# Kernel tuning notes

Hardware: AMD Instinct MI355X
Metric: run time of the kernel (lower is better)

## Reference

```python
import jax, jax.numpy as jnp
import numpy as np

T, B, S, H, E, V = 100, 64, 602, 1024, 512, 10000


def setup_inputs() -> dict:
    key = jax.random.key(0)
    ks = jax.random.split(key, 12)
    s = 0.02  # small init scale for numerical stability through tanh/sigmoid
    return {
        "tgt": jax.random.randint(ks[0], (T, B, 1), 0, V),
        "memory_bank": jax.random.normal(ks[1], (S, B, H), jnp.float32),
        "h0": jax.random.normal(ks[2], (2, B, H), jnp.float32) * 0.1,
        "c0": jax.random.normal(ks[3], (2, B, H), jnp.float32) * 0.1,
        "embedding": jax.random.normal(ks[4], (V, E), jnp.float32) * s,
        "Wi0": jax.random.normal(ks[5], (4 * H, E + H), jnp.float32) * s,
        "Wh0": jax.random.normal(ks[6], (4 * H, H), jnp.float32) * s,
        "bi0": jnp.zeros((4 * H,), jnp.float32),
        "bh0": jnp.zeros((4 * H,), jnp.float32),
        "Wi1": jax.random.normal(ks[7], (4 * H, H), jnp.float32) * s,
        "Wh1": jax.random.normal(ks[8], (4 * H, H), jnp.float32) * s,
        "bi1": jnp.zeros((4 * H,), jnp.float32),
        "bh1": jnp.zeros((4 * H,), jnp.float32),
        "W_attn": jax.random.normal(ks[9], (H, H), jnp.float32) * s,
        "W_out": jax.random.normal(ks[10], (H, 2 * H), jnp.float32) * s,
    }


def _lstm_cell(x, h, c, Wi, Wh, bi, bh):
    # PyTorch LSTM gate order: i, f, g, o
    g = x @ Wi.T + h @ Wh.T + bi + bh
    i, f, gg, o = jnp.split(g, 4, axis=-1)
    c2 = jax.nn.sigmoid(f) * c + jax.nn.sigmoid(i) * jnp.tanh(gg)
    h2 = jax.nn.sigmoid(o) * jnp.tanh(c2)
    return h2, c2


def reference(tgt, memory_bank, h0, c0, embedding, Wi0, Wh0, bi0, bh0,
              Wi1, Wh1, bi1, bh1, W_attn, W_out):
    emb = embedding[tgt[:, :, 0]]            # [T, B, E]
    M = jnp.transpose(memory_bank, (1, 0, 2))  # [B, S, H]

    def step(carry, e_t):
        hl0, hl1, cl0, cl1, feed = carry
        x = jnp.concatenate([e_t, feed], axis=-1)        # input feeding
        nh0, nc0 = _lstm_cell(x, hl0, cl0, Wi0, Wh0, bi0, bh0)
        nh1, nc1 = _lstm_cell(nh0, hl1, cl1, Wi1, Wh1, bi1, bh1)
        # GlobalAttention 'general': score = (h W) . m
        q = nh1 @ W_attn.T                                # [B, H]
        align = jnp.einsum('bh,bsh->bs', q, M)            # [B, S]
        a = jax.nn.softmax(align, axis=-1)
        ctx = jnp.einsum('bs,bsh->bh', a, M)              # [B, H]
        out = jnp.tanh(jnp.concatenate([ctx, nh1], -1) @ W_out.T)  # attn_h
        return (nh0, nh1, nc0, nc1, out), (out, a)

    init = (h0[0], h0[1], c0[0], c0[1], jnp.zeros((B, H), emb.dtype))
    (_, _, _, _, _), (outs, attns) = jax.lax.scan(step, init, emb)
    return outs, attns  # [T,B,H], [T,B,S]
```

## Files before the change

### kernel.cpp

```cpp
#include <hip/hip_runtime.h>


#define DI __device__ __forceinline__

typedef __attribute__((ext_vector_type(4))) short s4v;
typedef __attribute__((ext_vector_type(8))) short s8v;
typedef __attribute__((ext_vector_type(4))) float f4v;

DI float b2f(short u) {
  unsigned int x = ((unsigned int)(unsigned short)u) << 16;
  float f; __builtin_memcpy(&f, &x, 4); return f;
}
DI short f2b(float f) {
  unsigned int x; __builtin_memcpy(&x, &f, 4);
  return (short)((x + 0x7fffu + ((x >> 16) & 1u)) >> 16);
}
DI s8v cat8(s4v lo, s4v hi) {
  s8v r; r[0]=lo[0];r[1]=lo[1];r[2]=lo[2];r[3]=lo[3];
  r[4]=hi[0];r[5]=hi[1];r[6]=hi[2];r[7]=hi[3]; return r;
}
DI f4v mfma16(s8v a, s8v b, f4v c) {
  return __builtin_amdgcn_mfma_f32_16x16x32_bf16(a, b, c, 0, 0, 0);
}
DI float sigm(float x) { return 1.f / (1.f + __expf(-x)); }

DI unsigned long long ld64c(const void* p) {
  return __hip_atomic_load((const unsigned long long*)p, __ATOMIC_RELAXED,
                           __HIP_MEMORY_SCOPE_SYSTEM);
}
DI void st64c(void* p, unsigned long long v) {
  __hip_atomic_store((unsigned long long*)p, v, __ATOMIC_RELAXED,
                     __HIP_MEMORY_SCOPE_SYSTEM);
}
DI float ldfc(const float* p) {
  return __hip_atomic_load(p, __ATOMIC_RELAXED, __HIP_MEMORY_SCOPE_SYSTEM);
}
DI void stfc(float* p, float v) {
  __hip_atomic_store(p, v, __ATOMIC_RELAXED, __HIP_MEMORY_SCOPE_SYSTEM);
}
DI int ld32c(const int* p) {
  return __hip_atomic_load(p, __ATOMIC_RELAXED, __HIP_MEMORY_SCOPE_SYSTEM);
}
DI void st32c(int* p, int v) {
  __hip_atomic_store(p, v, __ATOMIC_RELAXED, __HIP_MEMORY_SCOPE_SYSTEM);
}
DI void st16c(short* p, short v) {
  asm volatile("global_store_short %0, %1, off sc0 sc1"
               :: "v"(p), "v"((unsigned int)(unsigned short)v) : "memory");
}
union U64S { unsigned long long u; short s[4]; };
union U64F { unsigned long long u; float f[2]; };


__global__ void cvt_bf16(const float* __restrict__ src, short* __restrict__ dst, long n8) {
  long i = (long)blockIdx.x * blockDim.x + threadIdx.x;
  long stride = (long)gridDim.x * blockDim.x;
  for (; i < n8; i += stride) {
    const float* s = src + i * 8;
    s8v o;
    #pragma unroll
    for (int j = 0; j < 8; ++j) o[j] = f2b(s[j]);
    *(s8v*)(dst + i * 8) = o;
  }
}

__global__ void pack_w(const float* __restrict__ WA, int Ka,
                       const float* __restrict__ WB, int Kb,
                       short* __restrict__ dst, int N, long total) {
  long i = (long)blockIdx.x * blockDim.x + threadIdx.x;
  long stride = (long)gridDim.x * blockDim.x;
  for (; i < total; i += stride) {
    int c = (int)(i & 3);
    long r = i >> 2;
    int n = (int)(r % N);
    int kt = (int)(r / N);
    int k = kt * 32 + c * 8;
    const float* s = (k < Ka) ? (WA + (size_t)n * Ka + k)
                              : (WB + (size_t)n * Kb + (k - Ka));
    s8v o;
    #pragma unroll
    for (int j = 0; j < 8; ++j) o[j] = f2b(s[j]);
    *(s8v*)(dst + r * 32 + c * 8) = o;
  }
}

__global__ __launch_bounds__(64) void emb_gather(const int* __restrict__ tgt,
                                                 const float* __restrict__ emb,
                                                 short* __restrict__ dst) {
  int tb = blockIdx.x;
  int idx = tgt[tb];
  const float* s = emb + (size_t)idx * 512 + threadIdx.x * 8;
  s8v o;
  #pragma unroll
  for (int j = 0; j < 8; ++j) o[j] = f2b(s[j]);
  *(s8v*)(dst + (size_t)tb * 512 + threadIdx.x * 8) = o;
}

__global__ void init_state(const float* __restrict__ h0, const float* __restrict__ c0,
                           short* __restrict__ h0r, short* __restrict__ h1r,
                           float* __restrict__ c0buf, float* __restrict__ c1buf,
                           short* __restrict__ feedr) {
  int i = blockIdx.x * 256 + threadIdx.x;
  if (i < 65536) {
    h0r[i] = f2b(h0[i]);
    h1r[i] = f2b(h0[65536 + i]);
    int row = i >> 10, col = i & 1023;
    size_t coff = (size_t)((row >> 4) * 64 + (col >> 4)) * 256
                + (row & 15) * 16 + (col & 15);
    c0buf[coff] = c0[i];
    c1buf[coff] = c0[65536 + i];
    feedr[i] = 0;
  }
}


template <int NG>
DI void kloop(const short* __restrict__ A, int ld, int nkt,
              const short* __restrict__ Wp, size_t wkt,
              f4v* acc, int rA, int g) {
  if (nkt <= 0) return;
  const short* ap = A + (size_t)rA * ld + 4 * g;
  s4v alo = *(const s4v*)ap, ahi = *(const s4v*)(ap + 16);
  s4v blo[NG], bhi[NG];
  #pragma unroll
  for (int t = 0; t < NG; ++t) {
    blo[t] = *(const s4v*)(Wp + (size_t)t * 32768);
    bhi[t] = *(const s4v*)(Wp + (size_t)t * 32768 + 16);
  }
  for (int kt = 0; kt < nkt - 1; ++kt) {
    const short* apn = ap + (kt + 1) * 32;
    const short* bpn = Wp + (size_t)(kt + 1) * wkt;
    s4v nalo = *(const s4v*)apn, nahi = *(const s4v*)(apn + 16);
    s4v nblo[NG], nbhi[NG];
    #pragma unroll
    for (int t = 0; t < NG; ++t) {
      nblo[t] = *(const s4v*)(bpn + (size_t)t * 32768);
      nbhi[t] = *(const s4v*)(bpn + (size_t)t * 32768 + 16);
    }
    s8v a = cat8(alo, ahi);
    #pragma unroll
    for (int t = 0; t < NG; ++t) acc[t] = mfma16(a, cat8(blo[t], bhi[t]), acc[t]);
    alo = nalo; ahi = nahi;
    #pragma unroll
    for (int t = 0; t < NG; ++t) { blo[t] = nblo[t]; bhi[t] = nbhi[t]; }
  }
  s8v a = cat8(alo, ahi);
  #pragma unroll
  for (int t = 0; t < NG; ++t) acc[t] = mfma16(a, cat8(blo[t], bhi[t]), acc[t]);
}

template <int NG>
DI void seg_gemm(const short* __restrict__ A0, int ld0, int n0,
                 const short* __restrict__ A1, int ld1, int n1,
                 const short* __restrict__ A2, int ld2, int n2,
                 const short* __restrict__ wbase, size_t wkt,
                 int k0, int k1, f4v* acc, int rA, int g) {
  int s = 0;
  {
    int a = k0 > s ? k0 : s, b = k1 < (s + n0) ? k1 : (s + n0);
    if (a < b) kloop<NG>(A0 + (size_t)(a - s) * 32, ld0, b - a,
                         wbase + (size_t)a * wkt, wkt, acc, rA, g);
    s += n0;
  }
  {
    int a = k0 > s ? k0 : s, b = k1 < (s + n1) ? k1 : (s + n1);
    if (a < b) kloop<NG>(A1 + (size_t)(a - s) * 32, ld1, b - a,
                         wbase + (size_t)a * wkt, wkt, acc, rA, g);
    s += n1;
  }
  if (n2 > 0) {
    int a = k0 > s ? k0 : s, b = k1 < (s + n2) ? k1 : (s + n2);
    if (a < b) kloop<NG>(A2 + (size_t)(a - s) * 32, ld2, b - a,
                         wbase + (size_t)a * wkt, wkt, acc, rA, g);
  }
}

template <int NG>
DI void wave_reduce(f4v* acc, float* smem, int w, int l) {
  #pragma unroll
  for (int t4 = 0; t4 < NG; ++t4)
    *(f4v*)&smem[(w * 64 + l) * 20 + t4 * 4] = acc[t4];
  __syncthreads();
  if (w == 0) {
    #pragma unroll
    for (int t4 = 0; t4 < NG; ++t4) {
      f4v s0 = *(f4v*)&smem[l * 20 + t4 * 4];
      #pragma unroll
      for (int ww = 1; ww < 4; ++ww) {
        f4v v = *(f4v*)&smem[(ww * 64 + l) * 20 + t4 * 4];
        #pragma unroll
        for (int j = 0; j < 4; ++j) s0[j] += v[j];
      }
      acc[t4] = s0;
    }
  }
}


DI void post(int* slot, int val) {
  if (threadIdx.x == 0) st32c(slot, val);
}
DI void wait64(const int* slots, int want) {
  for (;;) {
    int ok = 1;
    if (threadIdx.x < 64) ok = (ld32c(slots + threadIdx.x * 16) >= want);
    if (__syncthreads_and(ok)) break;
    __builtin_amdgcn_s_sleep(4);
  }
}
DI void wait4(const int* slots, int want) {
  for (;;) {
    int ok = 1;
    if (threadIdx.x < 4) ok = (ld32c(slots + threadIdx.x * 16) >= want);
    if (__syncthreads_and(ok)) break;
    __builtin_amdgcn_s_sleep(2);
  }
}


__global__ __launch_bounds__(256, 1) void decoder_k(
    const short* __restrict__ W0p, const short* __restrict__ W1p,
    const short* __restrict__ Wop, const short* __restrict__ Wap,
    const short* __restrict__ emba,
    const float* __restrict__ bi0, const float* __restrict__ bh0,
    const float* __restrict__ bi1, const float* __restrict__ bh1,
    short* h0r, short* h1r, short* feedr, short* ctxr, short* qb,
    float* c0b, float* c1b, float* alg, float* part, float* csum,
    const short* __restrict__ Mb, const float* __restrict__ memf,
    float* out, int useMb, int* bar) {
  __shared__ float smem[5248];
  const int bid = blockIdx.x, tid = threadIdx.x;
  const int w = tid >> 6, l = tid & 63, r15 = l & 15, g = l >> 4;
  const int cs = bid & 63, rt = bid >> 6;
  const int b = bid & 63, chunk = bid >> 6;
  int* s_p1 = bar;
  int* s_p2 = bar + 4096;
  int* s_p3 = bar + 8192;
  int* s_p6 = bar + 12288;
  int* s_p4 = bar + 16384;
  int* s_mg = bar + 20480;
  int* my_gemm_slot = bar ;
  f4v z = {0.f, 0.f, 0.f, 0.f};
  (void)my_gemm_slot;

  for (int t = 0; t < 100; ++t) {
    const size_t scur = (size_t)t * 65536, snxt = (size_t)(t + 1) * 65536;

    {
      wait64(s_p6 + rt * 1024, t);
      f4v acc[4] = {z, z, z, z};
      const short* wbase = W0p + (size_t)(cs * 16 + r15) * 32 + 4 * g;
      seg_gemm<4>(emba + (size_t)t * 64 * 512, 512, 16,
                  feedr + scur, 1024, 32, h0r + scur, 1024, 32,
                  wbase, (size_t)4096 * 32, w * 20, w * 20 + 20,
                  acc, rt * 16 + r15, g);
      wave_reduce<4>(acc, smem, w, l);
      if (w == 0) {
        int h = cs * 16 + r15;
        float bs0 = bi0[h] + bh0[h];
        float bs1 = bi0[1024 + h] + bh0[1024 + h];
        float bs2 = bi0[2048 + h] + bh0[2048 + h];
        float bs3 = bi0[3072 + h] + bh0[3072 + h];
        #pragma unroll
        for (int q = 0; q < 4; ++q) {
          int brow = rt * 16 + g * 4 + q;
          size_t off = (size_t)brow * 1024 + h;
          size_t coff = (size_t)bid * 256 + (g * 4 + q) * 16 + r15;
          float iv = acc[0][q] + bs0, fv = acc[1][q] + bs1;
          float gv = acc[2][q] + bs2, ov = acc[3][q] + bs3;
          float cn = sigm(fv) * c0b[coff] + sigm(iv) * tanhf(gv);
          float hn = sigm(ov) * tanhf(cn);
          c0b[coff] = cn;
          st16c(h0r + snxt + off, f2b(hn));
        }
      }
      __syncthreads();
      post(s_p1 + (rt * 64 + cs) * 16, t + 1);
    }

    {
      wait64(s_p1 + rt * 1024, t + 1);
      f4v acc[4] = {z, z, z, z};
      const short* wbase = W1p + (size_t)(cs * 16 + r15) * 32 + 4 * g;
      seg_gemm<4>(h0r + snxt, 1024, 32, h1r + scur, 1024, 32,
                  (const short*)nullptr, 0, 0,
                  wbase, (size_t)4096 * 32, w * 16, w * 16 + 16,
                  acc, rt * 16 + r15, g);
      wave_reduce<4>(acc, smem, w, l);
      if (w == 0) {
        int h = cs * 16 + r15;
        float bs0 = bi1[h] + bh1[h];
        float bs1 = bi1[1024 + h] + bh1[1024 + h];
        float bs2 = bi1[2048 + h] + bh1[2048 + h];
        float bs3 = bi1[3072 + h] + bh1[3072 + h];
        #pragma unroll
        for (int q = 0; q < 4; ++q) {
          int brow = rt * 16 + g * 4 + q;
          size_t off = (size_t)brow * 1024 + h;
          size_t coff = (size_t)bid * 256 + (g * 4 + q) * 16 + r15;
          float iv = acc[0][q] + bs0, fv = acc[1][q] + bs1;
          float gv = acc[2][q] + bs2, ov = acc[3][q] + bs3;
          float cn = sigm(fv) * c1b[coff] + sigm(iv) * tanhf(gv);
          float hn = sigm(ov) * tanhf(cn);
          c1b[coff] = cn;
          st16c(h1r + snxt + off, f2b(hn));
        }
      }
      __syncthreads();
      post(s_p2 + (rt * 64 + cs) * 16, t + 1);
    }

    {
      wait64(s_p2 + rt * 1024, t + 1);
      f4v acc[1] = {z};
      const short* wbase = Wap + (size_t)(cs * 16 + r15) * 32 + 4 * g;
      seg_gemm<1>(h1r + snxt, 1024, 32, (const short*)nullptr, 0, 0,
                  (const short*)nullptr, 0, 0,
                  wbase, (size_t)1024 * 32, w * 8, w * 8 + 8,
                  acc, rt * 16 + r15, g);
      wave_reduce<1>(acc, smem, w, l);
      if (w == 0) {
        int nb = cs * 16 + r15;
        #pragma unroll
        for (int q = 0; q < 4; ++q) {
          int brow = rt * 16 + g * 4 + q;
          st16c(qb + (size_t)brow * 1024 + nb, f2b(acc[0][q]));
        }
      }
      __syncthreads();
      post(s_p3 + (rt * 64 + cs) * 16, t + 1);
    }

    {
      wait64(s_p3 + (b >> 4) * 1024, t + 1);
      wait4(s_mg + b * 64, t);
      int s0 = chunk * 151;
      int send = 602 < s0 + 151 ? 602 : s0 + 151;
      const short* qp = qb + (size_t)b * 1024 + l * 16;
      float qf[16];
      #pragma unroll
      for (int c4 = 0; c4 < 4; ++c4) {
        U64S x; x.u = ld64c(qp + c4 * 4);
        #pragma unroll
        for (int j = 0; j < 4; ++j) qf[c4 * 4 + j] = b2f(x.s[j]);
      }
      float o[16];
      #pragma unroll
      for (int j = 0; j < 16; ++j) o[j] = 0.f;
      float ls8 = 0.f;
      for (int s = s0 + w; s < send; s += 16) {
        int sr[4] = {s, s + 4, s + 8, s + 12};
        bool has[4];
        #pragma unroll
        for (int r = 0; r < 4; ++r) has[r] = sr[r] < send;
        float mv[4][16];
        if (useMb) {
          #pragma unroll
          for (int r = 0; r < 4; ++r) {
            int sx = has[r] ? sr[r] : s;
            const short* mp = Mb + ((size_t)sx * 64 + b) * 1024 + l * 16;
            s8v a0 = *(const s8v*)mp, a1 = *(const s8v*)(mp + 8);
            #pragma unroll
            for (int j = 0; j < 8; ++j) {
              mv[r][j] = b2f(a0[j]); mv[r][8 + j] = b2f(a1[j]);
            }
          }
        } else {
          #pragma unroll
          for (int r = 0; r < 4; ++r) {
            int sx = has[r] ? sr[r] : s;
            const float* mp = memf + ((size_t)sx * 64 + b) * 1024 + l * 16;
            f4v a0 = *(const f4v*)mp, a1 = *(const f4v*)(mp + 4);
            f4v a2 = *(const f4v*)(mp + 8), a3 = *(const f4v*)(mp + 12);
            #pragma unroll
            for (int j = 0; j < 4; ++j) {
              mv[r][j] = a0[j]; mv[r][4 + j] = a1[j];
              mv[r][8 + j] = a2[j]; mv[r][12 + j] = a3[j];
            }
          }
        }
        float d[4] = {0.f, 0.f, 0.f, 0.f};
        #pragma unroll
        for (int j = 0; j < 16; ++j) {
          #pragma unroll
          for (int r = 0; r < 4; ++r) d[r] += qf[j] * mv[r][j];
        }
        #pragma unroll
        for (int off = 32; off; off >>= 1) {
          #pragma unroll
          for (int r = 0; r < 4; ++r) d[r] += __shfl_down(d[r], off);
        }
        float p[4];
        #pragma unroll
        for (int r = 0; r < 4; ++r) {
          d[r] = __shfl(d[r], 0);
          p[r] = has[r] ? __expf(fminf(d[r], 80.f) - 8.f) : 0.f;
          ls8 += p[r];
        }
        if (l == 0) {
          #pragma unroll
          for (int r = 0; r < 4; ++r)
            if (has[r]) stfc(alg + b * 602 + sr[r], p[r]);
        }
        #pragma unroll
        for (int j = 0; j < 16; ++j)
          o[j] += p[0] * mv[0][j] + p[1] * mv[1][j]
                + p[2] * mv[2][j] + p[3] * mv[3][j];
      }
      float* pp = part + (size_t)(b * 16 + chunk * 4 + w) * 1024;
      #pragma unroll
      for (int j4 = 0; j4 < 8; ++j4) {
        U64F x; x.f[0] = o[j4 * 2]; x.f[1] = o[j4 * 2 + 1];
        st64c(pp + l * 16 + j4 * 2, x.u);
      }
      if (l == 0) smem[5120 + w] = ls8;
      __syncthreads();
      if (tid == 0)
        stfc(csum + b * 4 + chunk,
             smem[5120] + smem[5121] + smem[5122] + smem[5123]);
      __syncthreads();
      post(s_p4 + (b * 4 + chunk) * 16, t + 1);
      wait4(s_p4 + b * 64, t + 1);
      {
        const float* cs4 = csum + b * 4;
        float L8 = ldfc(cs4) + ldfc(cs4 + 1) + ldfc(cs4 + 2) + ldfc(cs4 + 3);
        float invL = 1.f / L8;
        if (tid < 128) {
          int h = chunk * 256 + tid * 2;
          float a0 = 0.f, a1 = 0.f;
          #pragma unroll
          for (int p = 0; p < 16; ++p) {
            U64F x; x.u = ld64c(part + (size_t)(b * 16 + p) * 1024 + h);
            a0 += x.f[0]; a1 += x.f[1];
          }
          short* cp = ctxr + snxt + (size_t)b * 1024 + h;
          st16c(cp, f2b(a0 * invL));
          st16c(cp + 1, f2b(a1 * invL));
        }
        float* attns = out + 6553600 + (size_t)t * 64 * 602;
        for (int i = s0 + tid; i < send; i += 256)
          stfc(attns + b * 602 + i, ldfc(alg + b * 602 + i) * invL);
      }
      __syncthreads();
      post(s_mg + (b * 4 + chunk) * 16, t + 1);
    }

    {
      wait64(s_mg + rt * 1024, t + 1);
      f4v acc[1] = {z};
      const short* wbase = Wop + (size_t)(cs * 16 + r15) * 32 + 4 * g;
      seg_gemm<1>(ctxr + snxt, 1024, 32, h1r + snxt, 1024, 32,
                  (const short*)nullptr, 0, 0,
                  wbase, (size_t)1024 * 32, w * 16, w * 16 + 16,
                  acc, rt * 16 + r15, g);
      wave_reduce<1>(acc, smem, w, l);
      if (w == 0) {
        int nb = cs * 16 + r15;
        float* outp = out + (size_t)t * 65536;
        #pragma unroll
        for (int q = 0; q < 4; ++q) {
          int brow = rt * 16 + g * 4 + q;
          size_t off = (size_t)brow * 1024 + nb;
          float v = tanhf(acc[0][q]);
          stfc(outp + off, v);
          st16c(feedr + snxt + off, f2b(v));
        }
      }
      __syncthreads();
      post(s_p6 + (rt * 64 + cs) * 16, t + 1);
    }
  }
}


extern "C" void kernel_launch(void* const* d_in, const int* in_sizes, int n_in,
                              void* d_out, int out_size, void* d_ws, size_t ws_size,
                              hipStream_t stream) {
  const int*   tgt  = (const int*)  d_in[0];
  const float* mem  = (const float*)d_in[1];
  const float* h0   = (const float*)d_in[2];
  const float* c0   = (const float*)d_in[3];
  const float* embw = (const float*)d_in[4];
  const float* Wi0  = (const float*)d_in[5];
  const float* Wh0  = (const float*)d_in[6];
  const float* bi0  = (const float*)d_in[7];
  const float* bh0  = (const float*)d_in[8];
  const float* Wi1  = (const float*)d_in[9];
  const float* Wh1  = (const float*)d_in[10];
  const float* bi1  = (const float*)d_in[11];
  const float* bh1  = (const float*)d_in[12];
  const float* Wat  = (const float*)d_in[13];
  const float* Wou  = (const float*)d_in[14];
  float* out = (float*)d_out;

  char* base = (char*)d_ws;
  size_t off = 0;
  auto alloc = [&](size_t bytes) -> void* {
    void* p = base + off;
    off += (bytes + 255) & ~(size_t)255;
    return p;
  };
  const size_t RING = (size_t)101 * 65536;
  int* bar = (int*)alloc(131072);
  short* qb   = (short*)alloc(65536 * 2);
  float* csum = (float*)alloc(64 * 4 * 4);
  float* c0b  = (float*)alloc(65536 * 4);
  float* c1b  = (float*)alloc(65536 * 4);
  float* alg  = (float*)alloc((size_t)64 * 602 * 4);
  float* part = (float*)alloc((size_t)64 * 16 * 1024 * 4);
  short* emba = (short*)alloc((size_t)100 * 64 * 512 * 2);
  short* Wap  = (short*)alloc((size_t)32 * 1024 * 32 * 2);
  short* Wop  = (short*)alloc((size_t)64 * 1024 * 32 * 2);
  short* W1p  = (short*)alloc((size_t)64 * 4096 * 32 * 2);
  short* W0p  = (short*)alloc((size_t)80 * 4096 * 32 * 2);
  short* h0r  = (short*)alloc(RING * 2);
  short* h1r  = (short*)alloc(RING * 2);
  short* feedr= (short*)alloc(RING * 2);
  short* ctxr = (short*)alloc(RING * 2);
  const size_t MBE = (size_t)602 * 64 * 1024;
  bool useMb = (off + MBE * 2 + 256) <= ws_size;
  short* Mb = useMb ? (short*)alloc(MBE * 2) : nullptr;

  hipMemsetAsync(bar, 0, 131072, stream);
  hipLaunchKernelGGL(emb_gather, dim3(6400), dim3(64), 0, stream, tgt, embw, emba);
  hipLaunchKernelGGL(pack_w, dim3(2048), dim3(256), 0, stream, Wi0, 1536, Wh0, 1024,
                     W0p, 4096, (long)80 * 4096 * 4);
  hipLaunchKernelGGL(pack_w, dim3(2048), dim3(256), 0, stream, Wi1, 1024, Wh1, 1024,
                     W1p, 4096, (long)64 * 4096 * 4);
  hipLaunchKernelGGL(pack_w, dim3(1024), dim3(256), 0, stream, Wou, 2048, Wou, 2048,
                     Wop, 1024, (long)64 * 1024 * 4);
  hipLaunchKernelGGL(pack_w, dim3(512), dim3(256), 0, stream, Wat, 1024, Wat, 1024,
                     Wap, 1024, (long)32 * 1024 * 4);
  hipLaunchKernelGGL(init_state, dim3(256), dim3(256), 0, stream, h0, c0,
                     h0r, h1r, c0b, c1b, feedr);
  if (useMb)
    hipLaunchKernelGGL(cvt_bf16, dim3(2048), dim3(256), 0, stream, mem, Mb,
                       (long)(MBE / 8));

  hipLaunchKernelGGL(decoder_k, dim3(256), dim3(256), 0, stream,
                     W0p, W1p, Wop, Wap, emba,
                     bi0, bh0, bi1, bh1,
                     h0r, h1r, feedr, ctxr, qb,
                     c0b, c1b, alg, part, csum,
                     Mb, mem, out, (int)useMb,
                     bar);
}
```

Before: 7.353 ms.

## Stage GEMM epilogue outputs in LDS for 128-bit stores; dual-accumulator k-loop

```diff
diff --git a/kernel.cpp b/kernel.cpp
--- a/kernel.cpp
+++ b/kernel.cpp
@@ -47,6 +47,14 @@
 DI void st16c(short* p, short v) {
   asm volatile("global_store_short %0, %1, off sc0 sc1"
                :: "v"(p), "v"((unsigned int)(unsigned short)v) : "memory");
+}
+DI void st128c(void* p, s8v v) {
+  asm volatile("global_store_dwordx4 %0, %1, off sc0 sc1"
+               :: "v"(p), "v"(v) : "memory");
+}
+DI void st128cf(void* p, f4v v) {
+  asm volatile("global_store_dwordx4 %0, %1, off sc0 sc1"
+               :: "v"(p), "v"(v) : "memory");
 }
 union U64S { unsigned long long u; short s[4]; };
 union U64F { unsigned long long u; float f[2]; };
@@ -115,38 +123,44 @@
 
 
 template <int NG>
-DI void kloop(const short* __restrict__ A, int ld, int nkt,
-              const short* __restrict__ Wp, size_t wkt,
-              f4v* acc, int rA, int g) {
+DI void kloop_il(const short* __restrict__ A, int ld, int nkt,
+                 const short* __restrict__ Wp, size_t wkt,
+                 f4v* accA, f4v* accB, int rA, int g) {
   if (nkt <= 0) return;
   const short* ap = A + (size_t)rA * ld + 4 * g;
-  s4v alo = *(const s4v*)ap, ahi = *(const s4v*)(ap + 16);
-  s4v blo[NG], bhi[NG];
-  #pragma unroll
-  for (int t = 0; t < NG; ++t) {
-    blo[t] = *(const s4v*)(Wp + (size_t)t * 32768);
-    bhi[t] = *(const s4v*)(Wp + (size_t)t * 32768 + 16);
-  }
-  for (int kt = 0; kt < nkt - 1; ++kt) {
-    const short* apn = ap + (kt + 1) * 32;
-    const short* bpn = Wp + (size_t)(kt + 1) * wkt;
-    s4v nalo = *(const s4v*)apn, nahi = *(const s4v*)(apn + 16);
-    s4v nblo[NG], nbhi[NG];
+  int kt = 0;
+  for (; kt + 1 < nkt; kt += 2) {
+    const short* a0 = ap + kt * 32;
+    const short* a1 = ap + (kt + 1) * 32;
+    const short* b0 = Wp + (size_t)kt * wkt;
+    const short* b1 = Wp + (size_t)(kt + 1) * wkt;
+    s4v a0lo = *(const s4v*)a0, a0hi = *(const s4v*)(a0 + 16);
+    s4v a1lo = *(const s4v*)a1, a1hi = *(const s4v*)(a1 + 16);
+    s4v b0lo[NG], b0hi[NG], b1lo[NG], b1hi[NG];
     #pragma unroll
-    for (int t = 0; t < NG; ++t) {
-      nblo[t] = *(const s4v*)(bpn + (size_t)t * 32768);
-      nbhi[t] = *(const s4v*)(bpn + (size_t)t * 32768 + 16);
-    }
-    s8v a = cat8(alo, ahi);
+    for (int u = 0; u < NG; ++u) {
+      b0lo[u] = *(const s4v*)(b0 + (size_t)u * 32768);
+      b0hi[u] = *(const s4v*)(b0 + (size_t)u * 32768 + 16);
+      b1lo[u] = *(const s4v*)(b1 + (size_t)u * 32768);
+      b1hi[u] = *(const s4v*)(b1 + (size_t)u * 32768 + 16);
+    }
+    s8v aa = cat8(a0lo, a0hi), ab = cat8(a1lo, a1hi);
     #pragma unroll
-    for (int t = 0; t < NG; ++t) acc[t] = mfma16(a, cat8(blo[t], bhi[t]), acc[t]);
-    alo = nalo; ahi = nahi;
+    for (int u = 0; u < NG; ++u) {
+      accA[u] = mfma16(aa, cat8(b0lo[u], b0hi[u]), accA[u]);
+      accB[u] = mfma16(ab, cat8(b1lo[u], b1hi[u]), accB[u]);
+    }
+  }
+  if (kt < nkt) {
+    const short* a0 = ap + kt * 32;
+    const short* b0 = Wp + (size_t)kt * wkt;
+    s8v aa = cat8(*(const s4v*)a0, *(const s4v*)(a0 + 16));
     #pragma unroll
-    for (int t = 0; t < NG; ++t) { blo[t] = nblo[t]; bhi[t] = nbhi[t]; }
-  }
-  s8v a = cat8(alo, ahi);
-  #pragma unroll
-  for (int t = 0; t < NG; ++t) acc[t] = mfma16(a, cat8(blo[t], bhi[t]), acc[t]);
+    for (int u = 0; u < NG; ++u)
+      accA[u] = mfma16(aa, cat8(*(const s4v*)(b0 + (size_t)u * 32768),
+                                *(const s4v*)(b0 + (size_t)u * 32768 + 16)),
+                       accA[u]);
+  }
 }
 
 template <int NG>
@@ -154,24 +168,24 @@
                  const short* __restrict__ A1, int ld1, int n1,
                  const short* __restrict__ A2, int ld2, int n2,
                  const short* __restrict__ wbase, size_t wkt,
-                 int k0, int k1, f4v* acc, int rA, int g) {
+                 int k0, int k1, f4v* accA, f4v* accB, int rA, int g) {
   int s = 0;
   {
     int a = k0 > s ? k0 : s, b = k1 < (s + n0) ? k1 : (s + n0);
-    if (a < b) kloop<NG>(A0 + (size_t)(a - s) * 32, ld0, b - a,
-                         wbase + (size_t)a * wkt, wkt, acc, rA, g);
+    if (a < b) kloop_il<NG>(A0 + (size_t)(a - s) * 32, ld0, b - a,
+                            wbase + (size_t)a * wkt, wkt, accA, accB, rA, g);
     s += n0;
   }
   {
     int a = k0 > s ? k0 : s, b = k1 < (s + n1) ? k1 : (s + n1);
-    if (a < b) kloop<NG>(A1 + (size_t)(a - s) * 32, ld1, b - a,
-                         wbase + (size_t)a * wkt, wkt, acc, rA, g);
+    if (a < b) kloop_il<NG>(A1 + (size_t)(a - s) * 32, ld1, b - a,
+                            wbase + (size_t)a * wkt, wkt, accA, accB, rA, g);
     s += n1;
   }
   if (n2 > 0) {
     int a = k0 > s ? k0 : s, b = k1 < (s + n2) ? k1 : (s + n2);
-    if (a < b) kloop<NG>(A2 + (size_t)(a - s) * 32, ld2, b - a,
-                         wbase + (size_t)a * wkt, wkt, acc, rA, g);
+    if (a < b) kloop_il<NG>(A2 + (size_t)(a - s) * 32, ld2, b - a,
+                            wbase + (size_t)a * wkt, wkt, accA, accB, rA, g);
   }
 }
 
@@ -229,6 +243,8 @@
     const short* __restrict__ Mb, const float* __restrict__ memf,
     float* out, int useMb, int* bar) {
   __shared__ float smem[5248];
+  __shared__ __align__(16) short htile[256];
+  __shared__ __align__(16) float ftile[256];
   const int bid = blockIdx.x, tid = threadIdx.x;
   const int w = tid >> 6, l = tid & 63, r15 = l & 15, g = l >> 4;
   const int cs = bid & 63, rt = bid >> 6;
@@ -239,22 +255,24 @@
   int* s_p6 = bar + 12288;
   int* s_p4 = bar + 16384;
   int* s_mg = bar + 20480;
-  int* my_gemm_slot = bar ;
   f4v z = {0.f, 0.f, 0.f, 0.f};
-  (void)my_gemm_slot;
 
   for (int t = 0; t < 100; ++t) {
     const size_t scur = (size_t)t * 65536, snxt = (size_t)(t + 1) * 65536;
 
     {
       wait64(s_p6 + rt * 1024, t);
-      f4v acc[4] = {z, z, z, z};
+      f4v accA[4] = {z, z, z, z}, accB[4] = {z, z, z, z};
       const short* wbase = W0p + (size_t)(cs * 16 + r15) * 32 + 4 * g;
       seg_gemm<4>(emba + (size_t)t * 64 * 512, 512, 16,
                   feedr + scur, 1024, 32, h0r + scur, 1024, 32,
                   wbase, (size_t)4096 * 32, w * 20, w * 20 + 20,
-                  acc, rt * 16 + r15, g);
-      wave_reduce<4>(acc, smem, w, l);
+                  accA, accB, rt * 16 + r15, g);
+      #pragma unroll
+      for (int u = 0; u < 4; ++u)
+        #pragma unroll
+        for (int j = 0; j < 4; ++j) accA[u][j] += accB[u][j];
+      wave_reduce<4>(accA, smem, w, l);
       if (w == 0) {
         int h = cs * 16 + r15;
         float bs0 = bi0[h] + bh0[h];
@@ -263,16 +281,20 @@
         float bs3 = bi0[3072 + h] + bh0[3072 + h];
         #pragma unroll
         for (int q = 0; q < 4; ++q) {
-          int brow = rt * 16 + g * 4 + q;
-          size_t off = (size_t)brow * 1024 + h;
           size_t coff = (size_t)bid * 256 + (g * 4 + q) * 16 + r15;
-          float iv = acc[0][q] + bs0, fv = acc[1][q] + bs1;
-          float gv = acc[2][q] + bs2, ov = acc[3][q] + bs3;
+          float iv = accA[0][q] + bs0, fv = accA[1][q] + bs1;
+          float gv = accA[2][q] + bs2, ov = accA[3][q] + bs3;
           float cn = sigm(fv) * c0b[coff] + sigm(iv) * tanhf(gv);
           float hn = sigm(ov) * tanhf(cn);
           c0b[coff] = cn;
-          st16c(h0r + snxt + off, f2b(hn));
-        }
+          htile[(g * 4 + q) * 16 + r15] = f2b(hn);
+        }
+      }
+      __syncthreads();
+      if (tid < 32) {
+        int row = tid >> 1, c8 = (tid & 1) * 8;
+        st128c(h0r + snxt + (size_t)(rt * 16 + row) * 1024 + cs * 16 + c8,
+               *(const s8v*)&htile[row * 16 + c8]);
       }
       __syncthreads();
       post(s_p1 + (rt * 64 + cs) * 16, t + 1);
@@ -280,13 +302,17 @@
 
     {
       wait64(s_p1 + rt * 1024, t + 1);
-      f4v acc[4] = {z, z, z, z};
+      f4v accA[4] = {z, z, z, z}, accB[4] = {z, z, z, z};
       const short* wbase = W1p + (size_t)(cs * 16 + r15) * 32 + 4 * g;
       seg_gemm<4>(h0r + snxt, 1024, 32, h1r + scur, 1024, 32,
                   (const short*)nullptr, 0, 0,
                   wbase, (size_t)4096 * 32, w * 16, w * 16 + 16,
-                  acc, rt * 16 + r15, g);
-      wave_reduce<4>(acc, smem, w, l);
+                  accA, accB, rt * 16 + r15, g);
+      #pragma unroll
+      for (int u = 0; u < 4; ++u)
+        #pragma unroll
+        for (int j = 0; j < 4; ++j) accA[u][j] += accB[u][j];
+      wave_reduce<4>(accA, smem, w, l);
       if (w == 0) {
         int h = cs * 16 + r15;
         float bs0 = bi1[h] + bh1[h];
@@ -295,16 +321,20 @@
         float bs3 = bi1[3072 + h] + bh1[3072 + h];
         #pragma unroll
         for (int q = 0; q < 4; ++q) {
-          int brow = rt * 16 + g * 4 + q;
-          size_t off = (size_t)brow * 1024 + h;
           size_t coff = (size_t)bid * 256 + (g * 4 + q) * 16 + r15;
-          float iv = acc[0][q] + bs0, fv = acc[1][q] + bs1;
-          float gv = acc[2][q] + bs2, ov = acc[3][q] + bs3;
+          float iv = accA[0][q] + bs0, fv = accA[1][q] + bs1;
+          float gv = accA[2][q] + bs2, ov = accA[3][q] + bs3;
           float cn = sigm(fv) * c1b[coff] + sigm(iv) * tanhf(gv);
           float hn = sigm(ov) * tanhf(cn);
           c1b[coff] = cn;
-          st16c(h1r + snxt + off, f2b(hn));
-        }
+          htile[(g * 4 + q) * 16 + r15] = f2b(hn);
+        }
+      }
+      __syncthreads();
+      if (tid < 32) {
+        int row = tid >> 1, c8 = (tid & 1) * 8;
+        st128c(h1r + snxt + (size_t)(rt * 16 + row) * 1024 + cs * 16 + c8,
+               *(const s8v*)&htile[row * 16 + c8]);
       }
       __syncthreads();
       post(s_p2 + (rt * 64 + cs) * 16, t + 1);
@@ -312,20 +342,25 @@
 
     {
       wait64(s_p2 + rt * 1024, t + 1);
-      f4v acc[1] = {z};
+      f4v accA[1] = {z}, accB[1] = {z};
       const short* wbase = Wap + (size_t)(cs * 16 + r15) * 32 + 4 * g;
       seg_gemm<1>(h1r + snxt, 1024, 32, (const short*)nullptr, 0, 0,
                   (const short*)nullptr, 0, 0,
                   wbase, (size_t)1024 * 32, w * 8, w * 8 + 8,
-                  acc, rt * 16 + r15, g);
-      wave_reduce<1>(acc, smem, w, l);
+                  accA, accB, rt * 16 + r15, g);
+      #pragma unroll
+      for (int j = 0; j < 4; ++j) accA[0][j] += accB[0][j];
+      wave_reduce<1>(accA, smem, w, l);
       if (w == 0) {
-        int nb = cs * 16 + r15;
-        #pragma unroll
-        for (int q = 0; q < 4; ++q) {
-          int brow = rt * 16 + g * 4 + q;
-          st16c(qb + (size_t)brow * 1024 + nb, f2b(acc[0][q]));
-        }
+        #pragma unroll
+        for (int q = 0; q < 4; ++q)
+          htile[(g * 4 + q) * 16 + r15] = f2b(accA[0][q]);
+      }
+      __syncthreads();
+      if (tid < 32) {
+        int row = tid >> 1, c8 = (tid & 1) * 8;
+        st128c(qb + (size_t)(rt * 16 + row) * 1024 + cs * 16 + c8,
+               *(const s8v*)&htile[row * 16 + c8]);
       }
       __syncthreads();
       post(s_p3 + (rt * 64 + cs) * 16, t + 1);
@@ -447,24 +482,35 @@
 
     {
       wait64(s_mg + rt * 1024, t + 1);
-      f4v acc[1] = {z};
+      f4v accA[1] = {z}, accB[1] = {z};
       const short* wbase = Wop + (size_t)(cs * 16 + r15) * 32 + 4 * g;
       seg_gemm<1>(ctxr + snxt, 1024, 32, h1r + snxt, 1024, 32,
                   (const short*)nullptr, 0, 0,
                   wbase, (size_t)1024 * 32, w * 16, w * 16 + 16,
-                  acc, rt * 16 + r15, g);
-      wave_reduce<1>(acc, smem, w, l);
+                  accA, accB, rt * 16 + r15, g);
+      #pragma unroll
+      for (int j = 0; j < 4; ++j) accA[0][j] += accB[0][j];
+      wave_reduce<1>(accA, smem, w, l);
       if (w == 0) {
-        int nb = cs * 16 + r15;
-        float* outp = out + (size_t)t * 65536;
         #pragma unroll
         for (int q = 0; q < 4; ++q) {
-          int brow = rt * 16 + g * 4 + q;
-          size_t off = (size_t)brow * 1024 + nb;
-          float v = tanhf(acc[0][q]);
-          stfc(outp + off, v);
-          st16c(feedr + snxt + off, f2b(v));
-        }
+          float v = tanhf(accA[0][q]);
+          ftile[(g * 4 + q) * 16 + r15] = v;
+          htile[(g * 4 + q) * 16 + r15] = f2b(v);
+        }
+      }
+      __syncthreads();
+      if (tid < 32) {
+        int row = tid >> 1, c8 = (tid & 1) * 8;
+        st128c(feedr + snxt + (size_t)(rt * 16 + row) * 1024 + cs * 16 + c8,
+               *(const s8v*)&htile[row * 16 + c8]);
+      }
+      if (tid >= 64 && tid < 128) {
+        int x = tid - 64;
+        int row = x >> 2, c4 = (x & 3) * 4;
+        st128cf(out + (size_t)t * 65536 +
+                (size_t)(rt * 16 + row) * 1024 + cs * 16 + c4,
+                *(const f4v*)&ftile[row * 16 + c4]);
       }
       __syncthreads();
       post(s_p6 + (rt * 64 + cs) * 16, t + 1);
```

After: 7.306 ms (median of 2 runs). Within noise of the previous version (-0.6%).
